# Performance work log

Hardware: AMD Instinct MI355X
Metric: run time of the kernel (lower is better)

The kernel has to match this reference:

```python
import jax, jax.numpy as jnp
import numpy as np

EMBED = 1024
HEAD = 64

def setup_inputs() -> dict:
    key = jax.random.key(0)
    k1, k2, k3, k4 = jax.random.split(key, 4)
    x = jax.random.normal(k1, (8, 2048, EMBED), dtype=jnp.float32)
    # nn.Linear(E, H, bias=False) weights, stored as [E, H] for x @ W
    W_k = jax.random.normal(k2, (EMBED, HEAD), dtype=jnp.float32) * (EMBED ** -0.5)
    W_q = jax.random.normal(k3, (EMBED, HEAD), dtype=jnp.float32) * (EMBED ** -0.5)
    W_v = jax.random.normal(k4, (EMBED, HEAD), dtype=jnp.float32) * (EMBED ** -0.5)
    return {"x": x, "W_k": W_k, "W_q": W_q, "W_v": W_v}

def reference(x, W_k, W_q, W_v):
    B, T, E = x.shape
    keys = jnp.einsum('bte,eh->bth', x, W_k)
    queries = jnp.einsum('bte,eh->bth', x, W_q)
    values = jnp.einsum('bte,eh->bth', x, W_v)
    # NOTE: original scales by embedding size E, not head size
    scores = jnp.einsum('bqh,bkh->bqk', queries, keys) * (E ** -0.5)
    causal = jnp.tril(jnp.ones((T, T), dtype=bool))
    scores = jnp.where(causal, scores, -jnp.inf)
    weights = jax.nn.softmax(scores, axis=-1)
    return jnp.einsum('bqk,bkh->bqh', weights, values)
```

## Files before the change

kernel.cpp:

```cpp
#include <hip/hip_runtime.h>

typedef __attribute__((ext_vector_type(8))) short bf16x8;
typedef __attribute__((ext_vector_type(4))) float f32x4;
typedef __attribute__((ext_vector_type(4))) unsigned short u16x4;
typedef __attribute__((ext_vector_type(8))) unsigned short u16x8;
typedef __attribute__((ext_vector_type(4))) unsigned int u32x4;

#define MFMA(a, b, c) __builtin_amdgcn_mfma_f32_16x16x32_bf16(a, b, c, 0, 0, 0)

static __device__ __forceinline__ unsigned short f2bf(float x) {
    union { float f; unsigned u; } v; v.f = x;
    unsigned r = v.u + 0x7fffu + ((v.u >> 16) & 1u);
    return (unsigned short)(r >> 16);
}

static __device__ __forceinline__ bf16x8 pack_pa(
    float ea0, float ea1, float ea2, float ea3,
    float eb0, float eb1, float eb2, float eb3, bool odd)
{
    unsigned a1, a2, b1, b2;
    asm("v_cvt_pk_bf16_f32 %0, %1, %2" : "=v"(a1) : "v"(ea0), "v"(ea1));
    asm("v_cvt_pk_bf16_f32 %0, %1, %2" : "=v"(a2) : "v"(ea2), "v"(ea3));
    asm("v_cvt_pk_bf16_f32 %0, %1, %2" : "=v"(b1) : "v"(eb0), "v"(eb1));
    asm("v_cvt_pk_bf16_f32 %0, %1, %2" : "=v"(b2) : "v"(eb2), "v"(eb3));
    asm("v_permlane32_swap_b32 %0, %1" : "+v"(a1), "+v"(b1));
    asm("v_permlane32_swap_b32 %0, %1" : "+v"(a2), "+v"(b2));
    int sa1 = __shfl_xor((int)a1, 16);
    int sa2 = __shfl_xor((int)a2, 16);
    int sb1 = __shfl_xor((int)b1, 16);
    int sb2 = __shfl_xor((int)b2, 16);
    u32x4 paw;
    paw[0] = odd ? (unsigned)sb1 : a1;
    paw[1] = odd ? (unsigned)sb2 : a2;
    paw[2] = odd ? b1 : (unsigned)sa1;
    paw[3] = odd ? b2 : (unsigned)sa2;
    return __builtin_bit_cast(bf16x8, paw);
}

__global__ __launch_bounds__(256) void wtrans_k(
    const float* __restrict__ Wk, const float* __restrict__ Wq,
    const float* __restrict__ Wv, unsigned short* __restrict__ Wt)
{
    __shared__ float tl[64][65];
    const int w = blockIdx.x >> 4, kt = blockIdx.x & 15;
    const float* W = (w == 0) ? Wk : (w == 1) ? Wq : Wv;
    const int tid = threadIdx.x;
#pragma unroll
    for (int rep = 0; rep < 4; rep++) {
        int flat = rep * 256 + tid;
        int rr = flat >> 4, c4 = (flat & 15) * 4;
        f32x4 v = *(const f32x4*)(W + (kt * 64 + rr) * 64 + c4);
#pragma unroll
        for (int jj = 0; jj < 4; jj++) tl[c4 + jj][rr] = v[jj];
    }
    __syncthreads();
#pragma unroll
    for (int rep = 0; rep < 2; rep++) {
        int flat = rep * 256 + tid;
        int n = flat >> 3, k8 = (flat & 7) * 8;
        u16x8 h;
#pragma unroll
        for (int jj = 0; jj < 8; jj++) h[jj] = f2bf(tl[n][k8 + jj]);
        int grow = w * 64 + n;
        int gr = (k8 >> 3) ^ (grow & 7);
        *(u16x8*)(Wt + kt * 12288 + grow * 64 + gr * 8) = h;
    }
}

__global__ __launch_bounds__(256) void qkv_k(
    const float* __restrict__ x, const unsigned short* __restrict__ Wt,
    unsigned short* __restrict__ Qb, unsigned short* __restrict__ Kb,
    unsigned short* __restrict__ Vt)
{
    __shared__ __align__(16) unsigned short xl[2][64][72];
    __shared__ __align__(16) unsigned short wl[2][12288];
    const int tid = threadIdx.x;
    const int wid = tid >> 6, lane = tid & 63;
    const int lrow = lane & 15, g = lane >> 4;
    const int mbase = blockIdx.x * 64;
    const int msrow = (wid & 1) * 32;
    const int ntbase = (wid >> 1) * 6;

    const int xr0 = tid >> 4;
    const int xc16 = (tid & 15) * 4;
    const int wofs = tid * 8;

    const int swz0 = ((g    ) ^ (lrow & 7)) << 3;
    const int swz1 = ((g + 4) ^ (lrow & 7)) << 3;

    f32x4 acc0[6], acc1[6];
#pragma unroll
    for (int j = 0; j < 6; j++) {
        acc0[j] = (f32x4){0.f, 0.f, 0.f, 0.f};
        acc1[j] = (f32x4){0.f, 0.f, 0.f, 0.f};
    }

    f32x4 vx0, vx1, vx2, vx3;
    u16x8 rw0, rw1, rw2, rw3, rw4, rw5;
    {
        const float* xs = x + mbase * 1024 + xc16;
        vx0 = *(const f32x4*)(xs + (xr0     ) * 1024);
        vx1 = *(const f32x4*)(xs + (xr0 + 16) * 1024);
        vx2 = *(const f32x4*)(xs + (xr0 + 32) * 1024);
        vx3 = *(const f32x4*)(xs + (xr0 + 48) * 1024);
        const unsigned short* ws = Wt + wofs;
        rw0 = *(const u16x8*)(ws);
        rw1 = *(const u16x8*)(ws + 2048);
        rw2 = *(const u16x8*)(ws + 4096);
        rw3 = *(const u16x8*)(ws + 6144);
        rw4 = *(const u16x8*)(ws + 8192);
        rw5 = *(const u16x8*)(ws + 10240);
    }

#pragma unroll 1
    for (int t = 0; t < 16; ++t) {
        const int buf = t & 1;
        {
            unsigned d0, d1;
            unsigned* p;
            asm("v_cvt_pk_bf16_f32 %0, %1, %2" : "=v"(d0) : "v"(vx0[0]), "v"(vx0[1]));
            asm("v_cvt_pk_bf16_f32 %0, %1, %2" : "=v"(d1) : "v"(vx0[2]), "v"(vx0[3]));
            p = (unsigned*)&xl[buf][xr0][xc16];      p[0] = d0; p[1] = d1;
            asm("v_cvt_pk_bf16_f32 %0, %1, %2" : "=v"(d0) : "v"(vx1[0]), "v"(vx1[1]));
            asm("v_cvt_pk_bf16_f32 %0, %1, %2" : "=v"(d1) : "v"(vx1[2]), "v"(vx1[3]));
            p = (unsigned*)&xl[buf][xr0 + 16][xc16]; p[0] = d0; p[1] = d1;
            asm("v_cvt_pk_bf16_f32 %0, %1, %2" : "=v"(d0) : "v"(vx2[0]), "v"(vx2[1]));
            asm("v_cvt_pk_bf16_f32 %0, %1, %2" : "=v"(d1) : "v"(vx2[2]), "v"(vx2[3]));
            p = (unsigned*)&xl[buf][xr0 + 32][xc16]; p[0] = d0; p[1] = d1;
            asm("v_cvt_pk_bf16_f32 %0, %1, %2" : "=v"(d0) : "v"(vx3[0]), "v"(vx3[1]));
            asm("v_cvt_pk_bf16_f32 %0, %1, %2" : "=v"(d1) : "v"(vx3[2]), "v"(vx3[3]));
            p = (unsigned*)&xl[buf][xr0 + 48][xc16]; p[0] = d0; p[1] = d1;

            *(u16x8*)&wl[buf][wofs        ] = rw0;
            *(u16x8*)&wl[buf][wofs + 2048 ] = rw1;
            *(u16x8*)&wl[buf][wofs + 4096 ] = rw2;
            *(u16x8*)&wl[buf][wofs + 6144 ] = rw3;
            *(u16x8*)&wl[buf][wofs + 8192 ] = rw4;
            *(u16x8*)&wl[buf][wofs + 10240] = rw5;
        }
        if (t < 15) {
            const int kc = (t + 1) * 64;
            const float* xs = x + mbase * 1024 + kc + xc16;
            vx0 = *(const f32x4*)(xs + (xr0     ) * 1024);
            vx1 = *(const f32x4*)(xs + (xr0 + 16) * 1024);
            vx2 = *(const f32x4*)(xs + (xr0 + 32) * 1024);
            vx3 = *(const f32x4*)(xs + (xr0 + 48) * 1024);
            const unsigned short* ws = Wt + (t + 1) * 12288 + wofs;
            rw0 = *(const u16x8*)(ws);
            rw1 = *(const u16x8*)(ws + 2048);
            rw2 = *(const u16x8*)(ws + 4096);
            rw3 = *(const u16x8*)(ws + 6144);
            rw4 = *(const u16x8*)(ws + 8192);
            rw5 = *(const u16x8*)(ws + 10240);
        }
        __syncthreads();
#pragma unroll
        for (int ks = 0; ks < 2; ks++) {
            bf16x8 a0 = *(const bf16x8*)&xl[buf][msrow + lrow][ks * 32 + g * 8];
            bf16x8 a1 = *(const bf16x8*)&xl[buf][msrow + 16 + lrow][ks * 32 + g * 8];
            const int swz = ks ? swz1 : swz0;
#pragma unroll
            for (int j = 0; j < 6; j++) {
                int row = (ntbase + j) * 16 + lrow;
                bf16x8 b = *(const bf16x8*)&wl[buf][row * 64 + swz];
                acc0[j] = MFMA(a0, b, acc0[j]);
                acc1[j] = MFMA(a1, b, acc1[j]);
            }
        }
    }

#pragma unroll
    for (int j = 0; j < 6; j++) {
        int nt = ntbase + j;
        int w = nt >> 2;
        int col = (nt & 3) * 16 + lrow;
#pragma unroll
        for (int ms = 0; ms < 2; ms++) {
            const f32x4& a = ms ? acc1[j] : acc0[j];
            int r0 = mbase + msrow + ms * 16 + g * 4;
            if (w == 2) {
                int b = r0 >> 11, tt = r0 & 2047;
                u16x4 pv;
                pv[0] = f2bf(a[0]); pv[1] = f2bf(a[1]);
                pv[2] = f2bf(a[2]); pv[3] = f2bf(a[3]);
                *(u16x4*)(Vt + b * 131072 + col * 2048 + tt) = pv;
            } else {
                unsigned short* dst = (w == 0) ? Kb : Qb;
#pragma unroll
                for (int i = 0; i < 4; i++)
                    dst[(r0 + i) * 64 + col] = f2bf(a[i]);
            }
        }
    }
}

__global__ __launch_bounds__(256) void attn_k(
    const unsigned short* __restrict__ Qb, const unsigned short* __restrict__ Kb,
    const unsigned short* __restrict__ Vt, float* __restrict__ pO,
    float* __restrict__ pL)
{
    __shared__ __align__(16) unsigned short klds[2][64][64];
    __shared__ __align__(16) unsigned short vlds[2][64][64];
    const int tid = threadIdx.x;
    const int w = tid >> 6, lane = tid & 63;
    const int lrow = lane & 15, g = lane >> 4;
    const int bid = blockIdx.x;
    const int bandIdx = bid >> 5;
    const int batch = (bid >> 2) & 7;
    const int j = bid & 3;
    const int B = (bandIdx < 16) ? (31 - bandIdx) : (bandIdx - 16);

    const int qb  = B * 64;
    const int nch = B + 1;
    const int nc  = (nch > j) ? ((nch - j + 3) >> 2) : 0;

    const unsigned short* Kbase = Kb + batch * 2048 * 64;
    const unsigned short* Vbase = Vt + batch * 131072;
    const float C2 = 0.03125f * 1.44269504088896f;

    const int sr = tid >> 2;
    const int sc32 = tid & 3;
    const int sb0 = sr * 128 + (((sc32 * 2)     ^ (sr & 7)) << 4);
    const int sb1 = sr * 128 + (((sc32 * 2 + 1) ^ (sr & 7)) << 4);

    const int swz = (lrow & 7) << 4;
    const int rb0 = (lrow) * 128, rb1 = (16 + lrow) * 128,
              rb2 = (32 + lrow) * 128, rb3 = (48 + lrow) * 128;
    const int gk0 = (g << 4) ^ swz;
    const int gk1 = ((4 + g) << 4) ^ swz;
    const bool odd = (g & 1);

    const unsigned short* Qrow = Qb + (batch * 2048 + qb + w * 16 + lrow) * 64;
    bf16x8 q0 = *(const bf16x8*)(Qrow + g * 8);
    bf16x8 q1 = *(const bf16x8*)(Qrow + 32 + g * 8);
    const int qglob = qb + w * 16 + lrow;

    f32x4 o0 = {0.f,0.f,0.f,0.f}, o1 = o0, o2 = o0, o3 = o0;
    float lsum = 0.f;

    u16x8 rk0 = {}, rk1 = {}, rv0 = {}, rv1 = {};
    if (nc > 0) {
        const int kvb = j * 64;
        const unsigned short* ksrc = Kbase + (kvb + sr) * 64 + sc32 * 16;
        rk0 = *(const u16x8*)(ksrc); rk1 = *(const u16x8*)(ksrc + 8);
        const unsigned short* vsrc = Vbase + sr * 2048 + kvb + sc32 * 16;
        rv0 = *(const u16x8*)(vsrc); rv1 = *(const u16x8*)(vsrc + 8);
        char* kb = (char*)&klds[0][0][0];
        char* vb = (char*)&vlds[0][0][0];
        *(u16x8*)(kb + sb0) = rk0; *(u16x8*)(kb + sb1) = rk1;
        *(u16x8*)(vb + sb0) = rv0; *(u16x8*)(vb + sb1) = rv1;
    }
    __syncthreads();

    for (int idx = 0; idx < nc; ++idx) {
        const int c = j + idx * 4;
        const int cur = idx & 1;
        const int kvbase = c * 64;
        if (idx + 1 < nc) {
            const int kvb = kvbase + 256;
            const unsigned short* ksrc = Kbase + (kvb + sr) * 64 + sc32 * 16;
            rk0 = *(const u16x8*)(ksrc); rk1 = *(const u16x8*)(ksrc + 8);
            const unsigned short* vsrc = Vbase + sr * 2048 + kvb + sc32 * 16;
            rv0 = *(const u16x8*)(vsrc); rv1 = *(const u16x8*)(vsrc + 8);
        }

        const char* kb = (const char*)&klds[cur][0][0];
        const char* vb = (const char*)&vlds[cur][0][0];

        f32x4 t0 = {0.f,0.f,0.f,0.f}, t1 = t0, t2 = t0, t3 = t0;
        {
            bf16x8 a;
            a = *(const bf16x8*)(kb + rb0 + gk0); t0 = MFMA(a, q0, t0);
            a = *(const bf16x8*)(kb + rb0 + gk1); t0 = MFMA(a, q1, t0);
            a = *(const bf16x8*)(kb + rb1 + gk0); t1 = MFMA(a, q0, t1);
            a = *(const bf16x8*)(kb + rb1 + gk1); t1 = MFMA(a, q1, t1);
            a = *(const bf16x8*)(kb + rb2 + gk0); t2 = MFMA(a, q0, t2);
            a = *(const bf16x8*)(kb + rb2 + gk1); t2 = MFMA(a, q1, t2);
            a = *(const bf16x8*)(kb + rb3 + gk0); t3 = MFMA(a, q0, t3);
            a = *(const bf16x8*)(kb + rb3 + gk1); t3 = MFMA(a, q1, t3);
        }

        const bool maskc = (c == nch - 1);
        float eA[4], eB[4], eC[4], eD[4];
#pragma unroll
        for (int u = 0; u < 4; u++) {
            float v0 = t0[u] * C2, v1 = t1[u] * C2,
                  v2 = t2[u] * C2, v3 = t3[u] * C2;
            if (maskc) {
                int kvr = kvbase + g * 4 + u;
                v0 = (kvr      > qglob) ? -INFINITY : v0;
                v1 = (kvr + 16 > qglob) ? -INFINITY : v1;
                v2 = (kvr + 32 > qglob) ? -INFINITY : v2;
                v3 = (kvr + 48 > qglob) ? -INFINITY : v3;
            }
            eA[u] = __builtin_exp2f(v0);
            eB[u] = __builtin_exp2f(v1);
            eC[u] = __builtin_exp2f(v2);
            eD[u] = __builtin_exp2f(v3);
            lsum += (eA[u] + eB[u]) + (eC[u] + eD[u]);
        }

        bf16x8 pa0 = pack_pa(eA[0],eA[1],eA[2],eA[3], eB[0],eB[1],eB[2],eB[3], odd);
        bf16x8 pa1 = pack_pa(eC[0],eC[1],eC[2],eC[3], eD[0],eD[1],eD[2],eD[3], odd);

        {
            bf16x8 vv;
            vv = *(const bf16x8*)(vb + rb0 + gk0); o0 = MFMA(pa0, vv, o0);
            vv = *(const bf16x8*)(vb + rb0 + gk1); o0 = MFMA(pa1, vv, o0);
            vv = *(const bf16x8*)(vb + rb1 + gk0); o1 = MFMA(pa0, vv, o1);
            vv = *(const bf16x8*)(vb + rb1 + gk1); o1 = MFMA(pa1, vv, o1);
            vv = *(const bf16x8*)(vb + rb2 + gk0); o2 = MFMA(pa0, vv, o2);
            vv = *(const bf16x8*)(vb + rb2 + gk1); o2 = MFMA(pa1, vv, o2);
            vv = *(const bf16x8*)(vb + rb3 + gk0); o3 = MFMA(pa0, vv, o3);
            vv = *(const bf16x8*)(vb + rb3 + gk1); o3 = MFMA(pa1, vv, o3);
        }

        __syncthreads();
        if (idx + 1 < nc) {
            char* kw = (char*)&klds[cur ^ 1][0][0];
            char* vw = (char*)&vlds[cur ^ 1][0][0];
            *(u16x8*)(kw + sb0) = rk0; *(u16x8*)(kw + sb1) = rk1;
            *(u16x8*)(vw + sb0) = rv0; *(u16x8*)(vw + sb1) = rv1;
        }
        __syncthreads();
    }

    const int qrow0 = batch * 2048 + qb + w * 16;
    float* po = pO + ((size_t)j * 16384 + qrow0) * 64;
#pragma unroll
    for (int u = 0; u < 4; u++) {
        int r = (g * 4 + u) * 64;
        po[r +      lrow] = o0[u];
        po[r + 16 + lrow] = o1[u];
        po[r + 32 + lrow] = o2[u];
        po[r + 48 + lrow] = o3[u];
    }
    lsum += __shfl_xor(lsum, 16);
    lsum += __shfl_xor(lsum, 32);
    if (lane < 16) pL[j * 16384 + qrow0 + lane] = lsum;
}

__global__ __launch_bounds__(256) void comb_k(
    const float* __restrict__ pO, const float* __restrict__ pL,
    float* __restrict__ out)
{
    const int J = 16384 * 64;
    int id = blockIdx.x * 256 + threadIdx.x;
    int row = id >> 2, q = (id & 3) * 16;
    float inv = 1.f / (pL[row] + pL[16384 + row] + pL[32768 + row] + pL[49152 + row]);
    const float* p0 = pO + row * 64 + q;
    float* op = out + row * 64 + q;
#pragma unroll
    for (int k = 0; k < 4; k++) {
        f32x4 s = *(const f32x4*)(p0 + 4 * k)
                + *(const f32x4*)(p0 + J + 4 * k)
                + *(const f32x4*)(p0 + 2 * J + 4 * k)
                + *(const f32x4*)(p0 + 3 * J + 4 * k);
        *(f32x4*)(op + 4 * k) = s * inv;
    }
}

extern "C" void kernel_launch(void* const* d_in, const int* in_sizes, int n_in,
                              void* d_out, int out_size, void* d_ws, size_t ws_size,
                              hipStream_t stream) {
    const float* x  = (const float*)d_in[0];
    const float* Wk = (const float*)d_in[1];
    const float* Wq = (const float*)d_in[2];
    const float* Wv = (const float*)d_in[3];
    float* out = (float*)d_out;

    unsigned short* Wt = (unsigned short*)d_ws;
    unsigned short* Kb = Wt + 3 * 65536;
    unsigned short* Qb = Kb + 16384 * 64;
    unsigned short* Vt = Qb + 16384 * 64;
    float* pO = (float*)(Vt + 131072 * 8);
    float* pL = pO + 4 * 16384 * 64;

    wtrans_k<<<48, 256, 0, stream>>>(Wk, Wq, Wv, Wt);
    qkv_k<<<256, 256, 0, stream>>>(x, Wt, Qb, Kb, Vt);
    attn_k<<<1024, 256, 0, stream>>>(Qb, Kb, Vt, pO, pL);
    comb_k<<<256, 256, 0, stream>>>(pO, pL, out);
}
```

Before: 46.35 us.

## Deepen QKV projection prefetch to two stages with LDS-only barriers

Restructures the QKV projection main loop so that global loads of x and W are issued two K-chunks ahead into two register sets. The loop is unrolled by two with fixed LDS buffer indices, and each chunk's LDS write is placed after the MFMA block of the previous chunk. The full __syncthreads is replaced with a barrier that waits only on LDS counters, so in-flight global prefetches no longer stall the barrier. In exchange it uses more VGPRs for the second register set and issues redundant clamped loads past the last chunk.

```diff
diff --git a/kernel.cpp b/kernel.cpp
--- a/kernel.cpp
+++ b/kernel.cpp
@@ -12,6 +12,12 @@
     union { float f; unsigned u; } v; v.f = x;
     unsigned r = v.u + 0x7fffu + ((v.u >> 16) & 1u);
     return (unsigned short)(r >> 16);
+}
+
+static __device__ __forceinline__ void pub_barrier() {
+    asm volatile("s_waitcnt lgkmcnt(0)" ::: "memory");
+    __builtin_amdgcn_s_barrier();
+    asm volatile("" ::: "memory");
 }
 
 static __device__ __forceinline__ bf16x8 pack_pa(
@@ -67,6 +73,60 @@
     }
 }
 
+#define QKV_LOAD(C, X0, X1, X2, X3, W0, W1, W2, W3, W4, W5) do {          \
+        int c_ = (C) > 15 ? 15 : (C);                                     \
+        const float* xs_ = x + mbase * 1024 + c_ * 64 + xc16;             \
+        X0 = *(const f32x4*)(xs_ + (xr0     ) * 1024);                    \
+        X1 = *(const f32x4*)(xs_ + (xr0 + 16) * 1024);                    \
+        X2 = *(const f32x4*)(xs_ + (xr0 + 32) * 1024);                    \
+        X3 = *(const f32x4*)(xs_ + (xr0 + 48) * 1024);                    \
+        const unsigned short* ws_ = Wt + c_ * 12288 + wofs;               \
+        W0 = *(const u16x8*)(ws_);                                        \
+        W1 = *(const u16x8*)(ws_ + 2048);                                 \
+        W2 = *(const u16x8*)(ws_ + 4096);                                 \
+        W3 = *(const u16x8*)(ws_ + 6144);                                 \
+        W4 = *(const u16x8*)(ws_ + 8192);                                 \
+        W5 = *(const u16x8*)(ws_ + 10240);                                \
+    } while (0)
+
+#define QKV_WRITE(BUF, X0, X1, X2, X3, W0, W1, W2, W3, W4, W5) do {       \
+        unsigned d0_, d1_; unsigned* p_;                                  \
+        asm("v_cvt_pk_bf16_f32 %0, %1, %2" : "=v"(d0_) : "v"(X0[0]), "v"(X0[1])); \
+        asm("v_cvt_pk_bf16_f32 %0, %1, %2" : "=v"(d1_) : "v"(X0[2]), "v"(X0[3])); \
+        p_ = (unsigned*)&xl[BUF][xr0][xc16];      p_[0] = d0_; p_[1] = d1_; \
+        asm("v_cvt_pk_bf16_f32 %0, %1, %2" : "=v"(d0_) : "v"(X1[0]), "v"(X1[1])); \
+        asm("v_cvt_pk_bf16_f32 %0, %1, %2" : "=v"(d1_) : "v"(X1[2]), "v"(X1[3])); \
+        p_ = (unsigned*)&xl[BUF][xr0 + 16][xc16]; p_[0] = d0_; p_[1] = d1_; \
+        asm("v_cvt_pk_bf16_f32 %0, %1, %2" : "=v"(d0_) : "v"(X2[0]), "v"(X2[1])); \
+        asm("v_cvt_pk_bf16_f32 %0, %1, %2" : "=v"(d1_) : "v"(X2[2]), "v"(X2[3])); \
+        p_ = (unsigned*)&xl[BUF][xr0 + 32][xc16]; p_[0] = d0_; p_[1] = d1_; \
+        asm("v_cvt_pk_bf16_f32 %0, %1, %2" : "=v"(d0_) : "v"(X3[0]), "v"(X3[1])); \
+        asm("v_cvt_pk_bf16_f32 %0, %1, %2" : "=v"(d1_) : "v"(X3[2]), "v"(X3[3])); \
+        p_ = (unsigned*)&xl[BUF][xr0 + 48][xc16]; p_[0] = d0_; p_[1] = d1_; \
+        *(u16x8*)&wl[BUF][wofs        ] = W0;                             \
+        *(u16x8*)&wl[BUF][wofs + 2048 ] = W1;                             \
+        *(u16x8*)&wl[BUF][wofs + 4096 ] = W2;                             \
+        *(u16x8*)&wl[BUF][wofs + 6144 ] = W3;                             \
+        *(u16x8*)&wl[BUF][wofs + 8192 ] = W4;                             \
+        *(u16x8*)&wl[BUF][wofs + 10240] = W5;                             \
+    } while (0)
+
+#define QKV_MFMA(BUF) do {                                                \
+        _Pragma("unroll")                                                 \
+        for (int ks = 0; ks < 2; ks++) {                                  \
+            bf16x8 a0 = *(const bf16x8*)&xl[BUF][msrow + lrow][ks * 32 + g * 8];      \
+            bf16x8 a1 = *(const bf16x8*)&xl[BUF][msrow + 16 + lrow][ks * 32 + g * 8]; \
+            const int swz_ = ks ? swz1 : swz0;                            \
+            _Pragma("unroll")                                             \
+            for (int j = 0; j < 6; j++) {                                 \
+                int row_ = (ntbase + j) * 16 + lrow;                      \
+                bf16x8 b = *(const bf16x8*)&wl[BUF][row_ * 64 + swz_];    \
+                acc0[j] = MFMA(a0, b, acc0[j]);                           \
+                acc1[j] = MFMA(a1, b, acc1[j]);                           \
+            }                                                             \
+        }                                                                 \
+    } while (0)
+
 __global__ __launch_bounds__(256) void qkv_k(
     const float* __restrict__ x, const unsigned short* __restrict__ Wt,
     unsigned short* __restrict__ Qb, unsigned short* __restrict__ Kb,
@@ -95,78 +155,25 @@
         acc1[j] = (f32x4){0.f, 0.f, 0.f, 0.f};
     }
 
-    f32x4 vx0, vx1, vx2, vx3;
-    u16x8 rw0, rw1, rw2, rw3, rw4, rw5;
-    {
-        const float* xs = x + mbase * 1024 + xc16;
-        vx0 = *(const f32x4*)(xs + (xr0     ) * 1024);
-        vx1 = *(const f32x4*)(xs + (xr0 + 16) * 1024);
-        vx2 = *(const f32x4*)(xs + (xr0 + 32) * 1024);
-        vx3 = *(const f32x4*)(xs + (xr0 + 48) * 1024);
-        const unsigned short* ws = Wt + wofs;
-        rw0 = *(const u16x8*)(ws);
-        rw1 = *(const u16x8*)(ws + 2048);
-        rw2 = *(const u16x8*)(ws + 4096);
-        rw3 = *(const u16x8*)(ws + 6144);
-        rw4 = *(const u16x8*)(ws + 8192);
-        rw5 = *(const u16x8*)(ws + 10240);
-    }
+    f32x4 ax0, ax1, ax2, ax3;  u16x8 aw0, aw1, aw2, aw3, aw4, aw5;
+    f32x4 bx0, bx1, bx2, bx3;  u16x8 bw0, bw1, bw2, bw3, bw4, bw5;
+
+    QKV_LOAD(0, ax0, ax1, ax2, ax3, aw0, aw1, aw2, aw3, aw4, aw5);
+    QKV_LOAD(1, bx0, bx1, bx2, bx3, bw0, bw1, bw2, bw3, bw4, bw5);
+    QKV_WRITE(0, ax0, ax1, ax2, ax3, aw0, aw1, aw2, aw3, aw4, aw5);
+    QKV_LOAD(2, ax0, ax1, ax2, ax3, aw0, aw1, aw2, aw3, aw4, aw5);
+    pub_barrier();
 
 #pragma unroll 1
-    for (int t = 0; t < 16; ++t) {
-        const int buf = t & 1;
-        {
-            unsigned d0, d1;
-            unsigned* p;
-            asm("v_cvt_pk_bf16_f32 %0, %1, %2" : "=v"(d0) : "v"(vx0[0]), "v"(vx0[1]));
-            asm("v_cvt_pk_bf16_f32 %0, %1, %2" : "=v"(d1) : "v"(vx0[2]), "v"(vx0[3]));
-            p = (unsigned*)&xl[buf][xr0][xc16];      p[0] = d0; p[1] = d1;
-            asm("v_cvt_pk_bf16_f32 %0, %1, %2" : "=v"(d0) : "v"(vx1[0]), "v"(vx1[1]));
-            asm("v_cvt_pk_bf16_f32 %0, %1, %2" : "=v"(d1) : "v"(vx1[2]), "v"(vx1[3]));
-            p = (unsigned*)&xl[buf][xr0 + 16][xc16]; p[0] = d0; p[1] = d1;
-            asm("v_cvt_pk_bf16_f32 %0, %1, %2" : "=v"(d0) : "v"(vx2[0]), "v"(vx2[1]));
-            asm("v_cvt_pk_bf16_f32 %0, %1, %2" : "=v"(d1) : "v"(vx2[2]), "v"(vx2[3]));
-            p = (unsigned*)&xl[buf][xr0 + 32][xc16]; p[0] = d0; p[1] = d1;
-            asm("v_cvt_pk_bf16_f32 %0, %1, %2" : "=v"(d0) : "v"(vx3[0]), "v"(vx3[1]));
-            asm("v_cvt_pk_bf16_f32 %0, %1, %2" : "=v"(d1) : "v"(vx3[2]), "v"(vx3[3]));
-            p = (unsigned*)&xl[buf][xr0 + 48][xc16]; p[0] = d0; p[1] = d1;
-
-            *(u16x8*)&wl[buf][wofs        ] = rw0;
-            *(u16x8*)&wl[buf][wofs + 2048 ] = rw1;
-            *(u16x8*)&wl[buf][wofs + 4096 ] = rw2;
-            *(u16x8*)&wl[buf][wofs + 6144 ] = rw3;
-            *(u16x8*)&wl[buf][wofs + 8192 ] = rw4;
-            *(u16x8*)&wl[buf][wofs + 10240] = rw5;
-        }
-        if (t < 15) {
-            const int kc = (t + 1) * 64;
-            const float* xs = x + mbase * 1024 + kc + xc16;
-            vx0 = *(const f32x4*)(xs + (xr0     ) * 1024);
-            vx1 = *(const f32x4*)(xs + (xr0 + 16) * 1024);
-            vx2 = *(const f32x4*)(xs + (xr0 + 32) * 1024);
-            vx3 = *(const f32x4*)(xs + (xr0 + 48) * 1024);
-            const unsigned short* ws = Wt + (t + 1) * 12288 + wofs;
-            rw0 = *(const u16x8*)(ws);
-            rw1 = *(const u16x8*)(ws + 2048);
-            rw2 = *(const u16x8*)(ws + 4096);
-            rw3 = *(const u16x8*)(ws + 6144);
-            rw4 = *(const u16x8*)(ws + 8192);
-            rw5 = *(const u16x8*)(ws + 10240);
-        }
-        __syncthreads();
-#pragma unroll
-        for (int ks = 0; ks < 2; ks++) {
-            bf16x8 a0 = *(const bf16x8*)&xl[buf][msrow + lrow][ks * 32 + g * 8];
-            bf16x8 a1 = *(const bf16x8*)&xl[buf][msrow + 16 + lrow][ks * 32 + g * 8];
-            const int swz = ks ? swz1 : swz0;
-#pragma unroll
-            for (int j = 0; j < 6; j++) {
-                int row = (ntbase + j) * 16 + lrow;
-                bf16x8 b = *(const bf16x8*)&wl[buf][row * 64 + swz];
-                acc0[j] = MFMA(a0, b, acc0[j]);
-                acc1[j] = MFMA(a1, b, acc1[j]);
-            }
-        }
+    for (int t = 0; t < 16; t += 2) {
+        QKV_MFMA(0);
+        QKV_WRITE(1, bx0, bx1, bx2, bx3, bw0, bw1, bw2, bw3, bw4, bw5);
+        QKV_LOAD(t + 3, bx0, bx1, bx2, bx3, bw0, bw1, bw2, bw3, bw4, bw5);
+        pub_barrier();
+        QKV_MFMA(1);
+        QKV_WRITE(0, ax0, ax1, ax2, ax3, aw0, aw1, aw2, aw3, aw4, aw5);
+        QKV_LOAD(t + 4, ax0, ax1, ax2, ax3, aw0, aw1, aw2, aw3, aw4, aw5);
+        pub_barrier();
     }
 
 #pragma unroll
```

Measured after the change: 48.65 us. 5.0% more time.
